# Performance work log

Measured on AMD Instinct MI355X. Metric: run time of the kernel, lower is better.

## Reference

```python
import jax, jax.numpy as jnp
import numpy as np

D = 4096
N = 8192


def fwht(x):
    """Fast Walsh-Hadamard Transform (orthonormal, divided by sqrt(d)).

    log2(d) butterfly stages, each a single vectorized add/sub over the
    full tensor. Loop bound is static (log2 of trailing dim), jit-safe.
    """
    d = x.shape[-1]
    leading = x.shape[:-1]
    h = 1
    while h < d:
        x = x.reshape(*leading, d // (2 * h), 2, h)
        a = x[..., 0, :]
        b = x[..., 1, :]
        x = jnp.stack([a + b, a - b], axis=-2).reshape(*leading, d)
        h *= 2
    return x * jnp.asarray(d, x.dtype) ** -0.5


def setup_inputs() -> dict:
    key = jax.random.key(0)
    kx, ks = jax.random.split(key)
    x = jax.random.normal(kx, (N, D), dtype=jnp.float32)
    # deterministic random +/-1 sign vector (buffer of RHTRotation)
    signs = (jax.random.randint(ks, (D,), 0, 2).astype(jnp.float32) * 2.0 - 1.0)
    return {"x": x, "signs": signs}


def reference(x, signs):
    # randomized_hadamard: y = H @ (D x) / sqrt(d), D = diag(signs)
    return fwht(x * signs)
```

## Files before the change

kernel.cpp:

```cpp
#include <hip/hip_runtime.h>

#define D 4096
#define RPB 4

__device__ __forceinline__ void fwht16(float v[16]) {
#pragma unroll
    for (int s = 1; s < 16; s <<= 1) {
#pragma unroll
        for (int i = 0; i < 16; i++) {
            if (!(i & s)) {
                float a = v[i], b = v[i ^ s];
                v[i]     = a + b;
                v[i ^ s] = a - b;
            }
        }
    }
}

__device__ __forceinline__ void lds_barrier() {
    asm volatile("s_waitcnt lgkmcnt(0)" ::: "memory");
    __builtin_amdgcn_s_barrier();
}

__global__ __launch_bounds__(256, 6) void fwht_kernel(const float* __restrict__ x,
                                                      const float* __restrict__ signs,
                                                      float* __restrict__ out) {
    __shared__ float lds[4352];

    const int t = threadIdx.x;
    const long row0 = (long)blockIdx.x * RPB;

    float s[16];
    {
        const float4* __restrict__ sv = (const float4*)signs;
#pragma unroll
        for (int k = 0; k < 4; k++) {
            float4 g = sv[k * 256 + t];
            s[4 * k + 0] = g.x; s[4 * k + 1] = g.y;
            s[4 * k + 2] = g.z; s[4 * k + 3] = g.w;
        }
    }

    float v[16], u[16];

    {
        const float4* __restrict__ xv = (const float4*)(x + row0 * (long)D);
#pragma unroll
        for (int k = 0; k < 4; k++) {
            float4 a = xv[k * 256 + t];
            v[4 * k + 0] = a.x * s[4 * k + 0];
            v[4 * k + 1] = a.y * s[4 * k + 1];
            v[4 * k + 2] = a.z * s[4 * k + 2];
            v[4 * k + 3] = a.w * s[4 * k + 3];
        }
    }

    const int a2    = t >> 4, bb = t & 15;
    const int base2 = a2 * 272 + bb;
    const int p3    = (t >> 2) & 15;
    const int base3 = 17 * p3 + ((t >> 6) << 2) + (t & 3);
    const int outoff = (t >> 6) * 1024 + (t & 63);

    for (int i = 0; i < RPB; i++) {
        fwht16(v);
#pragma unroll
        for (int q = 0; q < 16; q++) lds[17 * t + q] = v[q];

        if (i + 1 < RPB) {
            const float4* __restrict__ xv =
                (const float4*)(x + (row0 + i + 1) * (long)D);
#pragma unroll
            for (int k = 0; k < 4; k++) {
                float4 a = xv[k * 256 + t];
                u[4 * k + 0] = a.x; u[4 * k + 1] = a.y;
                u[4 * k + 2] = a.z; u[4 * k + 3] = a.w;
            }
        }

        lds_barrier();

#pragma unroll
        for (int a1 = 0; a1 < 16; a1++) v[a1] = lds[base2 + a1 * 17];
        fwht16(v);
#pragma unroll
        for (int a1 = 0; a1 < 16; a1++) lds[base2 + a1 * 17] = v[a1];

        lds_barrier();

#pragma unroll
        for (int c = 0; c < 16; c++) v[c] = lds[base3 + c * 272];
        fwht16(v);
        {
            const float scale = 1.0f / 64.0f;
            float* __restrict__ orow = out + (row0 + i) * (long)D + outoff;
#pragma unroll
            for (int c = 0; c < 16; c++) orow[c * 64] = v[c] * scale;
        }

        if (i + 1 < RPB) {
            __builtin_amdgcn_s_barrier();
#pragma unroll
            for (int q = 0; q < 16; q++) v[q] = u[q] * s[q];
        }
    }
}

extern "C" void kernel_launch(void* const* d_in, const int* in_sizes, int n_in,
                              void* d_out, int out_size, void* d_ws, size_t ws_size,
                              hipStream_t stream) {
    const float* x = (const float*)d_in[0];
    const float* signs = (const float*)d_in[1];
    float* out = (float*)d_out;
    const int rows = in_sizes[0] / D;
    fwht_kernel<<<dim3(rows / RPB), dim3(256), 0, stream>>>(x, signs, out);
}
```

Measured before the change: 236.2 us.

## Use contiguous per-thread row chunks, halve rows per block, reload signs per row

Each thread now loads a contiguous 16-float chunk of the row (four adjacent float4s) instead of strided float4s. The LDS transpose indices and output mapping change so the last stage writes coalesced stride-256 scalar stores. Rows per block drop from 4 to 2, so twice as many blocks launch. The occupancy hint is removed and signs are reloaded from global each row rather than held in registers. This trades register pressure and occupancy for less well-coalesced input loads and more sign reloads.

Result: faster. 231.5 us (-2.0%).

```diff
diff --git a/kernel.cpp b/kernel.cpp
--- a/kernel.cpp
+++ b/kernel.cpp
@@ -1,7 +1,7 @@
 #include <hip/hip_runtime.h>
 
 #define D 4096
-#define RPB 4
+#define RPB 2
 
 __device__ __forceinline__ void fwht16(float v[16]) {
 #pragma unroll
@@ -17,91 +17,88 @@
     }
 }
 
-__device__ __forceinline__ void lds_barrier() {
+__device__ __forceinline__ void lgkm_barrier() {
     asm volatile("s_waitcnt lgkmcnt(0)" ::: "memory");
     __builtin_amdgcn_s_barrier();
+    asm volatile("" ::: "memory");
+}
+__device__ __forceinline__ void plain_barrier() {
+    asm volatile("" ::: "memory");
+    __builtin_amdgcn_s_barrier();
+    asm volatile("" ::: "memory");
 }
 
-__global__ __launch_bounds__(256, 6) void fwht_kernel(const float* __restrict__ x,
-                                                      const float* __restrict__ signs,
-                                                      float* __restrict__ out) {
+__global__ __launch_bounds__(256) void fwht_kernel(const float* __restrict__ x,
+                                                   const float* __restrict__ signs,
+                                                   float* __restrict__ out) {
     __shared__ float lds[4352];
 
     const int t = threadIdx.x;
     const long row0 = (long)blockIdx.x * RPB;
 
-    float s[16];
+    float v[16], u[16];
+
     {
-        const float4* __restrict__ sv = (const float4*)signs;
+        const float4* __restrict__ xv = (const float4*)(x + row0 * (long)D + t * 16);
 #pragma unroll
         for (int k = 0; k < 4; k++) {
-            float4 g = sv[k * 256 + t];
-            s[4 * k + 0] = g.x; s[4 * k + 1] = g.y;
-            s[4 * k + 2] = g.z; s[4 * k + 3] = g.w;
+            float4 a = xv[k];
+            u[4 * k + 0] = a.x; u[4 * k + 1] = a.y;
+            u[4 * k + 2] = a.z; u[4 * k + 3] = a.w;
         }
     }
 
-    float v[16], u[16];
+    const int base2 = (t >> 4) * 272 + (t & 15);
+    const int base3 = (t >> 4) * 17 + (t & 15);
 
-    {
-        const float4* __restrict__ xv = (const float4*)(x + row0 * (long)D);
 #pragma unroll
-        for (int k = 0; k < 4; k++) {
-            float4 a = xv[k * 256 + t];
-            v[4 * k + 0] = a.x * s[4 * k + 0];
-            v[4 * k + 1] = a.y * s[4 * k + 1];
-            v[4 * k + 2] = a.z * s[4 * k + 2];
-            v[4 * k + 3] = a.w * s[4 * k + 3];
+    for (int i = 0; i < RPB; i++) {
+        {
+            const float4* __restrict__ sv = (const float4*)(signs + t * 16);
+#pragma unroll
+            for (int k = 0; k < 4; k++) {
+                float4 s = sv[k];
+                v[4 * k + 0] = u[4 * k + 0] * s.x;
+                v[4 * k + 1] = u[4 * k + 1] * s.y;
+                v[4 * k + 2] = u[4 * k + 2] * s.z;
+                v[4 * k + 3] = u[4 * k + 3] * s.w;
+            }
         }
-    }
-
-    const int a2    = t >> 4, bb = t & 15;
-    const int base2 = a2 * 272 + bb;
-    const int p3    = (t >> 2) & 15;
-    const int base3 = 17 * p3 + ((t >> 6) << 2) + (t & 3);
-    const int outoff = (t >> 6) * 1024 + (t & 63);
-
-    for (int i = 0; i < RPB; i++) {
-        fwht16(v);
-#pragma unroll
-        for (int q = 0; q < 16; q++) lds[17 * t + q] = v[q];
 
         if (i + 1 < RPB) {
             const float4* __restrict__ xv =
-                (const float4*)(x + (row0 + i + 1) * (long)D);
+                (const float4*)(x + (row0 + i + 1) * (long)D + t * 16);
 #pragma unroll
             for (int k = 0; k < 4; k++) {
-                float4 a = xv[k * 256 + t];
+                float4 a = xv[k];
                 u[4 * k + 0] = a.x; u[4 * k + 1] = a.y;
                 u[4 * k + 2] = a.z; u[4 * k + 3] = a.w;
             }
         }
 
-        lds_barrier();
+        fwht16(v);
+#pragma unroll
+        for (int q = 0; q < 16; q++) lds[17 * t + q] = v[q];
+        lgkm_barrier();
 
 #pragma unroll
         for (int a1 = 0; a1 < 16; a1++) v[a1] = lds[base2 + a1 * 17];
         fwht16(v);
 #pragma unroll
         for (int a1 = 0; a1 < 16; a1++) lds[base2 + a1 * 17] = v[a1];
-
-        lds_barrier();
+        lgkm_barrier();
 
 #pragma unroll
-        for (int c = 0; c < 16; c++) v[c] = lds[base3 + c * 272];
+        for (int a2 = 0; a2 < 16; a2++) v[a2] = lds[base3 + a2 * 272];
         fwht16(v);
         {
             const float scale = 1.0f / 64.0f;
-            float* __restrict__ orow = out + (row0 + i) * (long)D + outoff;
+            float* __restrict__ orow = out + (row0 + i) * (long)D;
 #pragma unroll
-            for (int c = 0; c < 16; c++) orow[c * 64] = v[c] * scale;
+            for (int a2 = 0; a2 < 16; a2++) orow[a2 * 256 + t] = v[a2] * scale;
         }
 
-        if (i + 1 < RPB) {
-            __builtin_amdgcn_s_barrier();
-#pragma unroll
-            for (int q = 0; q < 16; q++) v[q] = u[q] * s[q];
-        }
+        if (i + 1 < RPB) plain_barrier();
     }
 }
 
```
